# Optimization experiments

Hardware: AMD Instinct MI355X
Metric: run time of the kernel (lower is better)

The kernel has to match this reference:

```python
import jax, jax.numpy as jnp
import numpy as np

EPS = 1e-8


def _similarity(feat):
    # feat: [b, c, h, w] -> pixel-pair cosine-similarity matrix [b, hw, hw]
    b, c, h, w = feat.shape
    feat = feat.astype(jnp.float32)
    # channel-wise L2 norm per pixel, eps added AFTER sqrt (matches torch code)
    norm = jnp.sqrt(jnp.sum(feat * feat, axis=1, keepdims=True)) + EPS  # [b,1,h,w]
    f = (feat / norm).reshape(b, c, h * w)                              # [b,c,hw]
    return jnp.einsum('icm,icn->imn', f, f)                             # [b,hw,hw]


def _sim_distance(feat1, feat2):
    b, _, h, w = feat1.shape
    hw = h * w
    sim_err = (_similarity(feat1) - _similarity(feat2)) ** 2 / (hw * hw) / b
    return jnp.sum(sim_err)


def setup_inputs() -> dict:
    key = jax.random.key(0)
    k1, k2, k3, k4 = jax.random.split(key, 4)
    return {
        'res1_t': jax.random.normal(k1, (4, 128, 64, 64), dtype=jnp.float32),
        'res1_s': jax.random.normal(k2, (4, 128, 64, 64), dtype=jnp.float32),
        'res2_t': jax.random.normal(k3, (4, 256, 32, 32), dtype=jnp.float32),
        'res2_s': jax.random.normal(k4, (4, 256, 32, 32), dtype=jnp.float32),
    }


def reference(res1_t, res1_s, res2_t, res2_s):
    # teacher features are detached in the original; forward math is identical
    pwl_g1 = _sim_distance(res1_t, res1_s)
    pwl_g2 = _sim_distance(res2_t, res2_s)
    loss = pwl_g1 + pwl_g2
    return (loss, jnp.stack([loss, pwl_g1, pwl_g2]))
```

## Files before the change

kernel.cpp:

```cpp
#include <hip/hip_runtime.h>
#include <math.h>

#define EPSF 1e-8f

typedef __attribute__((ext_vector_type(4))) short short4v;
typedef __attribute__((ext_vector_type(8))) short short8v;
typedef __attribute__((ext_vector_type(4))) float float4v;

__device__ inline short f2bf(float f) {
    unsigned u = __builtin_bit_cast(unsigned, f);
    unsigned r = (u + 0x7FFFu + ((u >> 16) & 1u)) >> 16;
    return (short)r;
}
__device__ inline float bf2f(short s) {
    unsigned u = ((unsigned)(unsigned short)s) << 16;
    return __builtin_bit_cast(float, u);
}

#define F1T 0
#define F1S 2097152
#define F2T 4194304
#define F2S 5242880

__constant__ int g1_tab[10][4] = {
    {0,0,0,1},{0,0,1,2},{0,1,1,1},
    {1,0,0,1},{1,0,1,2},{1,1,1,1},
    {2,0,0,-2},{2,0,1,-2},{2,1,0,-2},{2,1,1,-2},
};
__constant__ int g2_tab[36][4] = {
    {0,0,0,1},{0,0,1,2},{0,0,2,2},{0,0,3,2},{0,1,1,1},{0,1,2,2},{0,1,3,2},{0,2,2,1},{0,2,3,2},{0,3,3,1},
    {1,0,0,1},{1,0,1,2},{1,0,2,2},{1,0,3,2},{1,1,1,1},{1,1,2,2},{1,1,3,2},{1,2,2,1},{1,2,3,2},{1,3,3,1},
    {2,0,0,-2},{2,0,1,-2},{2,0,2,-2},{2,0,3,-2},
    {2,1,0,-2},{2,1,1,-2},{2,1,2,-2},{2,1,3,-2},
    {2,2,0,-2},{2,2,1,-2},{2,2,2,-2},{2,2,3,-2},
    {2,3,0,-2},{2,3,1,-2},{2,3,2,-2},{2,3,3,-2},
};

template<int C, int HW>
__device__ inline void prep_body(const float* __restrict__ x,
                                 short* __restrict__ f, int lp, int t)
{
    const int lanei = t & 7, slice = t >> 3;
    const int b = lp / HW, m = lp - b * HW;
    const float* p = x + (size_t)b * C * HW + m;
    short*       q = f + (size_t)b * C * HW + m;
    constexpr int CPR = C >> 5;
    short4v vals[CPR];
    float4 s0 = {0.f,0.f,0.f,0.f}, s1 = {0.f,0.f,0.f,0.f};
#pragma unroll
    for (int i = 0; i < CPR; i += 2) {
        float4 v0 = *(const float4*)(p + (size_t)(slice * CPR + i)     * HW);
        float4 v1 = *(const float4*)(p + (size_t)(slice * CPR + i + 1) * HW);
        s0.x += v0.x * v0.x; s0.y += v0.y * v0.y;
        s0.z += v0.z * v0.z; s0.w += v0.w * v0.w;
        s1.x += v1.x * v1.x; s1.y += v1.y * v1.y;
        s1.z += v1.z * v1.z; s1.w += v1.w * v1.w;
        vals[i]     = (short4v){ f2bf(v0.x), f2bf(v0.y), f2bf(v0.z), f2bf(v0.w) };
        vals[i + 1] = (short4v){ f2bf(v1.x), f2bf(v1.y), f2bf(v1.z), f2bf(v1.w) };
    }
    float4 s = { s0.x + s1.x, s0.y + s1.y, s0.z + s1.z, s0.w + s1.w };
    __shared__ float4 red[32][8];
    __shared__ float4 invl[8];
    red[slice][lanei] = s;
    __syncthreads();
    if (t < 8) {
        float4 tot = {0.f,0.f,0.f,0.f};
#pragma unroll
        for (int sl = 0; sl < 32; ++sl) {
            float4 v = red[sl][t];
            tot.x += v.x; tot.y += v.y; tot.z += v.z; tot.w += v.w;
        }
        invl[t] = (float4){ 1.f / (sqrtf(tot.x) + EPSF), 1.f / (sqrtf(tot.y) + EPSF),
                            1.f / (sqrtf(tot.z) + EPSF), 1.f / (sqrtf(tot.w) + EPSF) };
    }
    __syncthreads();
    const float4 iv = invl[lanei];
#pragma unroll
    for (int i = 0; i < CPR; ++i) {
        const int r = slice * CPR + i;
        short4v rv = vals[i];
        short4v o = { f2bf(bf2f(rv[0]) * iv.x), f2bf(bf2f(rv[1]) * iv.y),
                      f2bf(bf2f(rv[2]) * iv.z), f2bf(bf2f(rv[3]) * iv.w) };
        *(short4v*)(q + (size_t)r * HW) = o;
    }
}

__global__ __launch_bounds__(256) void prep_kernel(
    const float* __restrict__ x1t, const float* __restrict__ x1s,
    const float* __restrict__ x2t, const float* __restrict__ x2s,
    short* __restrict__ F, float* __restrict__ out)
{
    const int gp = blockIdx.x * 32;
    const int t = threadIdx.x;
    const int lanei = t & 7;
    if (blockIdx.x == 0 && t < 4) out[t] = 0.f;
    if (gp < 16384)
        prep_body<128, 4096>(x1t, F + F1T, gp + lanei * 4, t);
    else if (gp < 32768)
        prep_body<128, 4096>(x1s, F + F1S, gp - 16384 + lanei * 4, t);
    else if (gp < 36864)
        prep_body<256, 1024>(x2t, F + F2T, gp - 32768 + lanei * 4, t);
    else
        prep_body<256, 1024>(x2s, F + F2S, gp - 36864 + lanei * 4, t);
}

template<int HW, bool SHARE>
__device__ inline void gram_body(const short* __restrict__ Fa,
                                 const short* __restrict__ Fb,
                                 int k0, int lane, float4v (&acc)[4][4])
{
    const int r16 = lane & 15, quad = lane >> 4;
    const int kb = k0 + quad * 8;
#pragma unroll 1
    for (int it = 0; it < 4; ++it) {
        short8v af[4], bfr[4];
#pragma unroll
        for (int rt = 0; rt < 4; ++rt)
            af[rt] = *(const short8v*)(
                Fa + (size_t)(rt * 16 + r16) * HW + kb + it * 32);
        if (!SHARE) {
#pragma unroll
            for (int ct = 0; ct < 4; ++ct)
                bfr[ct] = *(const short8v*)(
                    Fb + (size_t)(ct * 16 + r16) * HW + kb + it * 32);
        }
#pragma unroll
        for (int rt = 0; rt < 4; ++rt)
#pragma unroll
            for (int ct = 0; ct < 4; ++ct)
                acc[rt][ct] = __builtin_amdgcn_mfma_f32_16x16x32_bf16(
                    af[rt], SHARE ? af[ct] : bfr[ct], acc[rt][ct], 0, 0, 0);
    }
}

__global__ __launch_bounds__(256, 4) void gramA_kernel(
    const short* __restrict__ F, float* __restrict__ partials)
{
    __shared__ float buf[2][64 * 68];

    const int id = blockIdx.x;
    const int t = threadIdx.x, w = t >> 6, lane = t & 63;
    const int r16 = lane & 15, quad = lane >> 4;

    float4v acc[4][4];
#pragma unroll
    for (int i = 0; i < 4; ++i)
#pragma unroll
        for (int j = 0; j < 4; ++j) acc[i][j] = (float4v){0.f, 0.f, 0.f, 0.f};

    if (id < 320) {
        const int comb = id >> 5, sub = id & 31;
        const int b = sub >> 3, ks = sub & 7;
        const int g = g1_tab[comb][0];
        const int ra = g1_tab[comb][1] << 6, rb = g1_tab[comb][2] << 6;
        const short* Fa = (g == 1 ? F + F1S : F + F1T) + (size_t)(b * 128 + ra) * 4096;
        const short* Fb = (g == 0 ? F + F1T : F + F1S) + (size_t)(b * 128 + rb) * 4096;
        const int k0 = ks * 512 + w * 128;
        if (g < 2 && ra == rb) gram_body<4096, true >(Fa, Fa, k0, lane, acc);
        else                   gram_body<4096, false>(Fa, Fb, k0, lane, acc);
    } else {
        const int id2 = id - 320;
        const int comb = id2 >> 3, sub = id2 & 7;
        const int b = sub >> 1, ks = sub & 1;
        const int g = g2_tab[comb][0];
        const int ra = g2_tab[comb][1] << 6, rb = g2_tab[comb][2] << 6;
        const short* Fa = (g == 1 ? F + F2S : F + F2T) + (size_t)(b * 256 + ra) * 1024;
        const short* Fb = (g == 0 ? F + F2T : F + F2S) + (size_t)(b * 256 + rb) * 1024;
        const int k0 = ks * 512 + w * 128;
        if (g < 2 && ra == rb) gram_body<1024, true >(Fa, Fa, k0, lane, acc);
        else                   gram_body<1024, false>(Fa, Fb, k0, lane, acc);
    }

#pragma unroll 1
    for (int rr = 0; rr < 2; ++rr) {
        if ((w >> 1) == rr) {
            float* dst = buf[w & 1];
#pragma unroll
            for (int rt = 0; rt < 4; ++rt)
#pragma unroll
                for (int ct = 0; ct < 4; ++ct)
#pragma unroll
                    for (int r = 0; r < 4; ++r) {
                        int off = (rt * 16 + quad * 4 + r) * 68 + ct * 16 + r16;
                        if (rr == 0) dst[off] = acc[rt][ct][r];
                        else         dst[off] += acc[rt][ct][r];
                    }
        }
        __syncthreads();
    }
    float* dst = partials + (size_t)id * 4096;
#pragma unroll
    for (int i = 0; i < 16; ++i) {
        int cell = (i << 8) + t;
        int off = (cell >> 6) * 68 + (cell & 63);
        dst[cell] = buf[0][off] + buf[1][off];
    }
}

template<int P>
__device__ inline float gramB_sum(const float* __restrict__ base, int t)
{
    float s = 0.f;
#pragma unroll
    for (int i = 0; i < 4; ++i) {
        const int c4 = i * 1024 + t * 4;
        float4 v = {0.f, 0.f, 0.f, 0.f};
#pragma unroll
        for (int p = 0; p < P; ++p) {
            float4 u = *(const float4*)(base + (size_t)p * 4096 + c4);
            v.x += u.x; v.y += u.y; v.z += u.z; v.w += u.w;
        }
        s += v.x * v.x + v.y * v.y + v.z * v.z + v.w * v.w;
    }
    return s;
}

__global__ __launch_bounds__(256) void gramB_kernel(
    const float* __restrict__ partials, float* __restrict__ out)
{
    __shared__ float scratch[256];
    const int tile = blockIdx.x, t = threadIdx.x;
    float s, wt; int which;
    if (tile < 40) {
        const int comb = tile >> 2, b = tile & 3;
        s = gramB_sum<8>(partials + (size_t)(comb * 32 + b * 8) * 4096, t);
        wt = (float)g1_tab[comb][3] * (1.0f / (4096.f * 4096.f * 4.f));
        which = 2;
    } else {
        const int t2 = tile - 40;
        const int comb = t2 >> 2, b = t2 & 3;
        s = gramB_sum<2>(partials + (size_t)(320 + comb * 8 + b * 2) * 4096, t);
        wt = (float)g2_tab[comb][3] * (1.0f / (1024.f * 1024.f * 4.f));
        which = 3;
    }
    s *= wt;
    scratch[t] = s;
    __syncthreads();
    for (int off = 128; off > 0; off >>= 1) {
        if (t < off) scratch[t] += scratch[t + off];
        __syncthreads();
    }
    if (t == 0) {
        float v = scratch[0];
        atomicAdd(&out[0], v);
        atomicAdd(&out[1], v);
        atomicAdd(&out[which], v);
    }
}

extern "C" void kernel_launch(void* const* d_in, const int* in_sizes, int n_in,
                              void* d_out, int out_size, void* d_ws, size_t ws_size,
                              hipStream_t stream)
{
    const float* x1t = (const float*)d_in[0];
    const float* x1s = (const float*)d_in[1];
    const float* x2t = (const float*)d_in[2];
    const float* x2s = (const float*)d_in[3];

    short* F        = (short*)d_ws;
    float* partials = (float*)d_ws + 3200000;

    prep_kernel<<<1280, 256, 0, stream>>>(x1t, x1s, x2t, x2s, F, (float*)d_out);
    gramA_kernel<<<608, 256, 0, stream>>>(F, partials);
    gramB_kernel<<<184, 256, 0, stream>>>(partials, (float*)d_out);
}
```

Measured before the change: 105.2 us.

## Fuse split-K Gram partials and reduction into a single full-K kernel

Replaces the split-K gramA kernel and the separate gramB reduction kernel with one gram_kernel. Each 512-thread block now covers the full K range of one 64x64 tile. Its 8 warps reduce the tile through shared memory, square and sum it, and then atomically add the result to the output. This drops the global partials buffer (write plus re-read) and one kernel launch. In exchange the grid shrinks to 184 blocks, which is fewer than the CU count, and each warp does a longer serial MFMA loop, so parallelism falls.

```diff
diff --git a/kernel.cpp b/kernel.cpp
--- a/kernel.cpp
+++ b/kernel.cpp
@@ -104,15 +104,15 @@
         prep_body<256, 1024>(x2s, F + F2S, gp - 36864 + lanei * 4, t);
 }
 
-template<int HW, bool SHARE>
-__device__ inline void gram_body(const short* __restrict__ Fa,
-                                 const short* __restrict__ Fb,
-                                 int k0, int lane, float4v (&acc)[4][4])
+template<int HW, int ITERS, bool SHARE>
+__device__ inline void gram_accum(const short* __restrict__ Fa,
+                                  const short* __restrict__ Fb,
+                                  int k0, int lane, float4v (&acc)[4][4])
 {
     const int r16 = lane & 15, quad = lane >> 4;
     const int kb = k0 + quad * 8;
-#pragma unroll 1
-    for (int it = 0; it < 4; ++it) {
+#pragma unroll 2
+    for (int it = 0; it < ITERS; ++it) {
         short8v af[4], bfr[4];
 #pragma unroll
         for (int rt = 0; rt < 4; ++rt)
@@ -133,10 +133,11 @@
     }
 }
 
-__global__ __launch_bounds__(256, 4) void gramA_kernel(
-    const short* __restrict__ F, float* __restrict__ partials)
+__global__ __launch_bounds__(512, 2) void gram_kernel(
+    const short* __restrict__ F, float* __restrict__ out)
 {
     __shared__ float buf[2][64 * 68];
+    __shared__ float scratch[8];
 
     const int id = blockIdx.x;
     const int t = threadIdx.x, w = t >> 6, lane = t & 63;
@@ -148,31 +149,34 @@
 #pragma unroll
         for (int j = 0; j < 4; ++j) acc[i][j] = (float4v){0.f, 0.f, 0.f, 0.f};
 
-    if (id < 320) {
-        const int comb = id >> 5, sub = id & 31;
-        const int b = sub >> 3, ks = sub & 7;
+    float wt; int which;
+    if (id < 40) {
+        const int comb = id >> 2, b = id & 3;
         const int g = g1_tab[comb][0];
         const int ra = g1_tab[comb][1] << 6, rb = g1_tab[comb][2] << 6;
         const short* Fa = (g == 1 ? F + F1S : F + F1T) + (size_t)(b * 128 + ra) * 4096;
         const short* Fb = (g == 0 ? F + F1T : F + F1S) + (size_t)(b * 128 + rb) * 4096;
-        const int k0 = ks * 512 + w * 128;
-        if (g < 2 && ra == rb) gram_body<4096, true >(Fa, Fa, k0, lane, acc);
-        else                   gram_body<4096, false>(Fa, Fb, k0, lane, acc);
+        const int k0 = w * 512;
+        if (g < 2 && ra == rb) gram_accum<4096, 16, true >(Fa, Fa, k0, lane, acc);
+        else                   gram_accum<4096, 16, false>(Fa, Fb, k0, lane, acc);
+        wt = (float)g1_tab[comb][3] * (1.0f / (4096.f * 4096.f * 4.f));
+        which = 2;
     } else {
-        const int id2 = id - 320;
-        const int comb = id2 >> 3, sub = id2 & 7;
-        const int b = sub >> 1, ks = sub & 1;
+        const int id2 = id - 40;
+        const int comb = id2 >> 2, b = id2 & 3;
         const int g = g2_tab[comb][0];
         const int ra = g2_tab[comb][1] << 6, rb = g2_tab[comb][2] << 6;
         const short* Fa = (g == 1 ? F + F2S : F + F2T) + (size_t)(b * 256 + ra) * 1024;
         const short* Fb = (g == 0 ? F + F2T : F + F2S) + (size_t)(b * 256 + rb) * 1024;
-        const int k0 = ks * 512 + w * 128;
-        if (g < 2 && ra == rb) gram_body<1024, true >(Fa, Fa, k0, lane, acc);
-        else                   gram_body<1024, false>(Fa, Fb, k0, lane, acc);
+        const int k0 = w * 128;
+        if (g < 2 && ra == rb) gram_accum<1024, 4, true >(Fa, Fa, k0, lane, acc);
+        else                   gram_accum<1024, 4, false>(Fa, Fb, k0, lane, acc);
+        wt = (float)g2_tab[comb][3] * (1.0f / (1024.f * 1024.f * 4.f));
+        which = 3;
     }
 
 #pragma unroll 1
-    for (int rr = 0; rr < 2; ++rr) {
+    for (int rr = 0; rr < 4; ++rr) {
         if ((w >> 1) == rr) {
             float* dst = buf[w & 1];
 #pragma unroll
@@ -188,60 +192,23 @@
         }
         __syncthreads();
     }
-    float* dst = partials + (size_t)id * 4096;
-#pragma unroll
-    for (int i = 0; i < 16; ++i) {
-        int cell = (i << 8) + t;
+
+    float s = 0.f;
+#pragma unroll
+    for (int i = 0; i < 8; ++i) {
+        int cell = (i << 9) + t;
         int off = (cell >> 6) * 68 + (cell & 63);
-        dst[cell] = buf[0][off] + buf[1][off];
-    }
-}
-
-template<int P>
-__device__ inline float gramB_sum(const float* __restrict__ base, int t)
-{
-    float s = 0.f;
-#pragma unroll
-    for (int i = 0; i < 4; ++i) {
-        const int c4 = i * 1024 + t * 4;
-        float4 v = {0.f, 0.f, 0.f, 0.f};
-#pragma unroll
-        for (int p = 0; p < P; ++p) {
-            float4 u = *(const float4*)(base + (size_t)p * 4096 + c4);
-            v.x += u.x; v.y += u.y; v.z += u.z; v.w += u.w;
-        }
-        s += v.x * v.x + v.y * v.y + v.z * v.z + v.w * v.w;
-    }
-    return s;
-}
-
-__global__ __launch_bounds__(256) void gramB_kernel(
-    const float* __restrict__ partials, float* __restrict__ out)
-{
-    __shared__ float scratch[256];
-    const int tile = blockIdx.x, t = threadIdx.x;
-    float s, wt; int which;
-    if (tile < 40) {
-        const int comb = tile >> 2, b = tile & 3;
-        s = gramB_sum<8>(partials + (size_t)(comb * 32 + b * 8) * 4096, t);
-        wt = (float)g1_tab[comb][3] * (1.0f / (4096.f * 4096.f * 4.f));
-        which = 2;
-    } else {
-        const int t2 = tile - 40;
-        const int comb = t2 >> 2, b = t2 & 3;
-        s = gramB_sum<2>(partials + (size_t)(320 + comb * 8 + b * 2) * 4096, t);
-        wt = (float)g2_tab[comb][3] * (1.0f / (1024.f * 1024.f * 4.f));
-        which = 3;
+        float v = buf[0][off] + buf[1][off];
+        s += v * v;
     }
     s *= wt;
-    scratch[t] = s;
+#pragma unroll
+    for (int off = 32; off > 0; off >>= 1) s += __shfl_down(s, off);
+    if (lane == 0) scratch[w] = s;
     __syncthreads();
-    for (int off = 128; off > 0; off >>= 1) {
-        if (t < off) scratch[t] += scratch[t + off];
-        __syncthreads();
-    }
     if (t == 0) {
-        float v = scratch[0];
+        float v = scratch[0] + scratch[1] + scratch[2] + scratch[3]
+                + scratch[4] + scratch[5] + scratch[6] + scratch[7];
         atomicAdd(&out[0], v);
         atomicAdd(&out[1], v);
         atomicAdd(&out[which], v);
@@ -257,10 +224,8 @@
     const float* x2t = (const float*)d_in[2];
     const float* x2s = (const float*)d_in[3];
 
-    short* F        = (short*)d_ws;
-    float* partials = (float*)d_ws + 3200000;
+    short* F = (short*)d_ws;
 
     prep_kernel<<<1280, 256, 0, stream>>>(x1t, x1s, x2t, x2s, F, (float*)d_out);
-    gramA_kernel<<<608, 256, 0, stream>>>(F, partials);
-    gramB_kernel<<<184, 256, 0, stream>>>(partials, (float*)d_out);
-}
+    gram_kernel<<<184, 512, 0, stream>>>(F, (float*)d_out);
+}
```

Measured after the change: 122.7 us. 1.17x slower.

## Stage Gram tiles through LDS and split output tile across waves

Applied to the files above, without the earlier changes.

The Gram kernel now stages 64x128 slices of A and B through shared memory with register prefetch of the next K slice. Each wave computes a 32x32 quadrant of the 64x64 output over the full K range, instead of every wave computing the full tile over its own K slice. This removes the cross-wave LDS reduction and cuts per-wave register accumulators from 16 to 4 MFMA tiles. In exchange it adds two barriers per K step and extra LDS traffic.

```diff
diff --git a/kernel.cpp b/kernel.cpp
--- a/kernel.cpp
+++ b/kernel.cpp
@@ -104,49 +104,90 @@
         prep_body<256, 1024>(x2s, F + F2S, gp - 36864 + lanei * 4, t);
 }
 
+#define LSTR 136
+
 template<int HW, bool SHARE>
-__device__ inline void gram_body(const short* __restrict__ Fa,
+__device__ inline void gram_tile(const short* __restrict__ Fa,
                                  const short* __restrict__ Fb,
-                                 int k0, int lane, float4v (&acc)[4][4])
-{
+                                 int k0, int t,
+                                 short* __restrict__ ldsA,
+                                 short* __restrict__ ldsB,
+                                 float4v (&acc)[2][2])
+{
+    const int lane = t & 63, w = t >> 6;
     const int r16 = lane & 15, quad = lane >> 4;
-    const int kb = k0 + quad * 8;
+    const int srow = t >> 4, skc = t & 15;
+    const int rt2 = (w >> 1) * 2, ct2 = (w & 1) * 2;
+
+    short8v ar[4], br[4];
+#pragma unroll
+    for (int p = 0; p < 4; ++p)
+        ar[p] = *(const short8v*)(Fa + (size_t)(p * 16 + srow) * HW + k0 + skc * 8);
+    if (!SHARE) {
+#pragma unroll
+        for (int p = 0; p < 4; ++p)
+            br[p] = *(const short8v*)(Fb + (size_t)(p * 16 + srow) * HW + k0 + skc * 8);
+    }
+
 #pragma unroll 1
-    for (int it = 0; it < 4; ++it) {
-        short8v af[4], bfr[4];
-#pragma unroll
-        for (int rt = 0; rt < 4; ++rt)
-            af[rt] = *(const short8v*)(
-                Fa + (size_t)(rt * 16 + r16) * HW + kb + it * 32);
+    for (int st = 0; st < 4; ++st) {
+#pragma unroll
+        for (int p = 0; p < 4; ++p)
+            *(short8v*)(ldsA + (p * 16 + srow) * LSTR + skc * 8) = ar[p];
         if (!SHARE) {
 #pragma unroll
-            for (int ct = 0; ct < 4; ++ct)
-                bfr[ct] = *(const short8v*)(
-                    Fb + (size_t)(ct * 16 + r16) * HW + kb + it * 32);
-        }
-#pragma unroll
-        for (int rt = 0; rt < 4; ++rt)
-#pragma unroll
-            for (int ct = 0; ct < 4; ++ct)
-                acc[rt][ct] = __builtin_amdgcn_mfma_f32_16x16x32_bf16(
-                    af[rt], SHARE ? af[ct] : bfr[ct], acc[rt][ct], 0, 0, 0);
+            for (int p = 0; p < 4; ++p)
+                *(short8v*)(ldsB + (p * 16 + srow) * LSTR + skc * 8) = br[p];
+        }
+        __syncthreads();
+        if (st < 3) {
+            const int k1 = k0 + (st + 1) * 128;
+#pragma unroll
+            for (int p = 0; p < 4; ++p)
+                ar[p] = *(const short8v*)(Fa + (size_t)(p * 16 + srow) * HW + k1 + skc * 8);
+            if (!SHARE) {
+#pragma unroll
+                for (int p = 0; p < 4; ++p)
+                    br[p] = *(const short8v*)(Fb + (size_t)(p * 16 + srow) * HW + k1 + skc * 8);
+            }
+        }
+        const short* A = ldsA;
+        const short* B = SHARE ? ldsA : ldsB;
+#pragma unroll
+        for (int ks = 0; ks < 4; ++ks) {
+            short8v af[2], bf[2];
+#pragma unroll
+            for (int i = 0; i < 2; ++i)
+                af[i] = *(const short8v*)(A + ((rt2 + i) * 16 + r16) * LSTR + ks * 32 + quad * 8);
+#pragma unroll
+            for (int j = 0; j < 2; ++j)
+                bf[j] = *(const short8v*)(B + ((ct2 + j) * 16 + r16) * LSTR + ks * 32 + quad * 8);
+#pragma unroll
+            for (int i = 0; i < 2; ++i)
+#pragma unroll
+                for (int j = 0; j < 2; ++j)
+                    acc[i][j] = __builtin_amdgcn_mfma_f32_16x16x32_bf16(
+                        af[i], bf[j], acc[i][j], 0, 0, 0);
+        }
+        __syncthreads();
     }
 }
 
 __global__ __launch_bounds__(256, 4) void gramA_kernel(
     const short* __restrict__ F, float* __restrict__ partials)
 {
-    __shared__ float buf[2][64 * 68];
+    __shared__ __align__(16) short ldsA[64 * LSTR];
+    __shared__ __align__(16) short ldsB[64 * LSTR];
 
     const int id = blockIdx.x;
     const int t = threadIdx.x, w = t >> 6, lane = t & 63;
     const int r16 = lane & 15, quad = lane >> 4;
 
-    float4v acc[4][4];
-#pragma unroll
-    for (int i = 0; i < 4; ++i)
-#pragma unroll
-        for (int j = 0; j < 4; ++j) acc[i][j] = (float4v){0.f, 0.f, 0.f, 0.f};
+    float4v acc[2][2];
+#pragma unroll
+    for (int i = 0; i < 2; ++i)
+#pragma unroll
+        for (int j = 0; j < 2; ++j) acc[i][j] = (float4v){0.f, 0.f, 0.f, 0.f};
 
     if (id < 320) {
         const int comb = id >> 5, sub = id & 31;
@@ -155,9 +196,9 @@
         const int ra = g1_tab[comb][1] << 6, rb = g1_tab[comb][2] << 6;
         const short* Fa = (g == 1 ? F + F1S : F + F1T) + (size_t)(b * 128 + ra) * 4096;
         const short* Fb = (g == 0 ? F + F1T : F + F1S) + (size_t)(b * 128 + rb) * 4096;
-        const int k0 = ks * 512 + w * 128;
-        if (g < 2 && ra == rb) gram_body<4096, true >(Fa, Fa, k0, lane, acc);
-        else                   gram_body<4096, false>(Fa, Fb, k0, lane, acc);
+        const int k0 = ks * 512;
+        if (g < 2 && ra == rb) gram_tile<4096, true >(Fa, Fa, k0, t, ldsA, ldsB, acc);
+        else                   gram_tile<4096, false>(Fa, Fb, k0, t, ldsA, ldsB, acc);
     } else {
         const int id2 = id - 320;
         const int comb = id2 >> 3, sub = id2 & 7;
@@ -166,35 +207,21 @@
         const int ra = g2_tab[comb][1] << 6, rb = g2_tab[comb][2] << 6;
         const short* Fa = (g == 1 ? F + F2S : F + F2T) + (size_t)(b * 256 + ra) * 1024;
         const short* Fb = (g == 0 ? F + F2T : F + F2S) + (size_t)(b * 256 + rb) * 1024;
-        const int k0 = ks * 512 + w * 128;
-        if (g < 2 && ra == rb) gram_body<1024, true >(Fa, Fa, k0, lane, acc);
-        else                   gram_body<1024, false>(Fa, Fb, k0, lane, acc);
-    }
-
-#pragma unroll 1
-    for (int rr = 0; rr < 2; ++rr) {
-        if ((w >> 1) == rr) {
-            float* dst = buf[w & 1];
-#pragma unroll
-            for (int rt = 0; rt < 4; ++rt)
-#pragma unroll
-                for (int ct = 0; ct < 4; ++ct)
-#pragma unroll
-                    for (int r = 0; r < 4; ++r) {
-                        int off = (rt * 16 + quad * 4 + r) * 68 + ct * 16 + r16;
-                        if (rr == 0) dst[off] = acc[rt][ct][r];
-                        else         dst[off] += acc[rt][ct][r];
-                    }
-        }
-        __syncthreads();
-    }
+        const int k0 = ks * 512;
+        if (g < 2 && ra == rb) gram_tile<1024, true >(Fa, Fa, k0, t, ldsA, ldsB, acc);
+        else                   gram_tile<1024, false>(Fa, Fb, k0, t, ldsA, ldsB, acc);
+    }
+
     float* dst = partials + (size_t)id * 4096;
-#pragma unroll
-    for (int i = 0; i < 16; ++i) {
-        int cell = (i << 8) + t;
-        int off = (cell >> 6) * 68 + (cell & 63);
-        dst[cell] = buf[0][off] + buf[1][off];
-    }
+    const int rt2 = (w >> 1) * 2, ct2 = (w & 1) * 2;
+#pragma unroll
+    for (int i = 0; i < 2; ++i)
+#pragma unroll
+        for (int j = 0; j < 2; ++j)
+#pragma unroll
+            for (int r = 0; r < 4; ++r)
+                dst[((rt2 + i) * 16 + quad * 4 + r) * 64 + (ct2 + j) * 16 + r16]
+                    = acc[i][j][r];
 }
 
 template<int P>
```

After: 91.49 us. 1.15x faster.
